# Performance work log

Hardware: AMD Instinct MI355X
Metric: run time of the kernel (lower is better)

The kernel has to match this reference:

```python
import jax, jax.numpy as jnp
import numpy as np

N = 50000
E = 800000
IN_DIM = 256
HID = 32
HEADS = 4
OUT_DIM = 40
NEG_SLOPE = 0.2


def gat_layer(x, src, dst, W, a_src, a_dst, b, n_nodes, heads, ch, concat):
    # x: [N, F_in], W: [F_in, heads*ch], a_src/a_dst: [heads, ch], b: [out]
    h = (x @ W).reshape(n_nodes, heads, ch)                 # [N,H,C]
    alpha_s = jnp.einsum('nhc,hc->nh', h, a_src)            # [N,H]
    alpha_d = jnp.einsum('nhc,hc->nh', h, a_dst)            # [N,H]
    e = jax.nn.leaky_relu(alpha_s[src] + alpha_d[dst], NEG_SLOPE)  # [E,H]
    # segment softmax over destination neighborhoods (self-loops guarantee nonempty)
    m = jax.ops.segment_max(e, dst, num_segments=n_nodes)   # [N,H]
    e = jnp.exp(e - m[dst])
    denom = jax.ops.segment_sum(e, dst, num_segments=n_nodes)
    alpha = e / (denom[dst] + 1e-16)                         # [E,H]
    msg = h[src] * alpha[:, :, None]                         # [E,H,C]
    out = jax.ops.segment_sum(msg, dst, num_segments=n_nodes)  # [N,H,C]
    out = out.reshape(n_nodes, heads * ch) if concat else out.mean(axis=1)
    return out + b


def setup_inputs() -> dict:
    key = jax.random.key(0)
    ks = jax.random.split(key, 10)
    x = jax.random.normal(ks[0], (N, IN_DIM), dtype=jnp.float32)
    edge_index = jax.random.randint(ks[1], (2, E), 0, N, dtype=jnp.int32)
    s1 = 1.0 / np.sqrt(IN_DIM)
    s2 = 1.0 / np.sqrt(HID * HEADS)
    return {
        'x': x,
        'edge_index': edge_index,
        'W1': jax.random.normal(ks[2], (IN_DIM, HEADS * HID), dtype=jnp.float32) * s1,
        'a_src1': jax.random.normal(ks[3], (HEADS, HID), dtype=jnp.float32) * s1,
        'a_dst1': jax.random.normal(ks[4], (HEADS, HID), dtype=jnp.float32) * s1,
        'b1': jnp.zeros((HEADS * HID,), dtype=jnp.float32),
        'W2': jax.random.normal(ks[5], (HEADS * HID, OUT_DIM), dtype=jnp.float32) * s2,
        'a_src2': jax.random.normal(ks[6], (1, OUT_DIM), dtype=jnp.float32) * s2,
        'a_dst2': jax.random.normal(ks[7], (1, OUT_DIM), dtype=jnp.float32) * s2,
        'b2': jnp.zeros((OUT_DIM,), dtype=jnp.float32),
    }


def reference(x, edge_index, W1, a_src1, a_dst1, b1, W2, a_src2, a_dst2, b2):
    # PyG GATConv adds self-loops by default
    loops = jnp.arange(N, dtype=edge_index.dtype)
    src = jnp.concatenate([edge_index[0], loops])
    dst = jnp.concatenate([edge_index[1], loops])
    h = gat_layer(x, src, dst, W1, a_src1, a_dst1, b1, N, HEADS, HID, True)
    h = jax.nn.relu(h)
    out = gat_layer(h, src, dst, W2, a_src2, a_dst2, b2, N, 1, OUT_DIM, False)
    return jax.nn.log_softmax(out, axis=1)
```

## Files before the change

### kernel.cpp

```cpp
#include <hip/hip_runtime.h>
#include <math.h>

#define N_NODES 50000
#define N_EDGES 800000
#define IN_DIM  256
#define F1      128
#define HEADS   4
#define OUT_DIM 40
#define NEG     0.2f

#define NB   391
#define CAP  3072
#define EB   4096
#define PREW 16
#define G1B  782

typedef __attribute__((ext_vector_type(8))) short short8;
typedef __attribute__((ext_vector_type(4))) float float4v;

__device__ __forceinline__ unsigned short f2bf(float f) {
  unsigned int u = __float_as_uint(f);
  u += 0x7FFF + ((u >> 16) & 1);
  return (unsigned short)(u >> 16);
}
__device__ __forceinline__ float bf2f(unsigned short h) {
  return __uint_as_float((unsigned int)h << 16);
}
__device__ __forceinline__ float bflo(unsigned int u) { return __uint_as_float(u << 16); }
__device__ __forceinline__ float bfhi(unsigned int u) { return __uint_as_float(u & 0xffff0000u); }

__device__ __forceinline__ float lrelu(float e) { return e > 0.f ? e : e * NEG; }

__device__ __forceinline__ void gload_lds16(const void* g, void* l) {
  __builtin_amdgcn_global_load_lds(
      (const __attribute__((address_space(1))) unsigned int*)g,
      (__attribute__((address_space(3))) unsigned int*)l, 16, 0, 0);
}

__global__ __launch_bounds__(256) void pre_kernel(const float* __restrict__ W1,
                                                  unsigned short* __restrict__ wHi,
                                                  unsigned short* __restrict__ wLo,
                                                  const int* __restrict__ ei,
                                                  int* __restrict__ gcnt,
                                                  int2* __restrict__ gbucket) {
  __shared__ int smem[EB * 2 + NB * 3];
  if (blockIdx.x < PREW) {
    int tid = blockIdx.x * 256 + threadIdx.x;
    int kk = tid >> 9;
    int rest = tid & 511;
    int t = rest >> 6;
    int lane = rest & 63;
    int q = lane >> 4;
    int ln = lane & 15;
    int n = t * 16 + ln;
    unsigned int hi[4], lo[4];
#pragma unroll
    for (int jj = 0; jj < 4; jj++) {
      unsigned short h0, h1, l0, l1;
      {
        float v = W1[(kk * 32 + q * 8 + jj * 2) * F1 + n];
        h0 = f2bf(v); l0 = f2bf(v - bf2f(h0));
      }
      {
        float v = W1[(kk * 32 + q * 8 + jj * 2 + 1) * F1 + n];
        h1 = f2bf(v); l1 = f2bf(v - bf2f(h1));
      }
      hi[jj] = (unsigned int)h0 | ((unsigned int)h1 << 16);
      lo[jj] = (unsigned int)l0 | ((unsigned int)l1 << 16);
    }
    size_t base = (size_t)tid * 8;
    *(uint4*)&wHi[base] = make_uint4(hi[0], hi[1], hi[2], hi[3]);
    *(uint4*)&wLo[base] = make_uint4(lo[0], lo[1], lo[2], lo[3]);
  } else {
    int* ls = smem;
    int* ld = smem + EB;
    int* lcnt = smem + 2 * EB;
    int* lcur = lcnt + NB;
    int* gbaseS = lcur + NB;
    int tid = threadIdx.x;
    size_t base = (size_t)(blockIdx.x - PREW) * EB;
    for (int t = tid; t < NB; t += 256) { lcnt[t] = 0; lcur[t] = 0; }
    __syncthreads();
#pragma unroll
    for (int l = 0; l < EB / 256; l++) {
      int li = l * 256 + tid;
      size_t idx = base + li;
      int s = 0, d = -1;
      if (idx < N_EDGES) {
        s = ei[idx];
        d = ei[N_EDGES + idx];
        atomicAdd(&lcnt[d >> 7], 1);
      }
      ls[li] = s;
      ld[li] = d;
    }
    __syncthreads();
    for (int t = tid; t < NB; t += 256) gbaseS[t] = atomicAdd(&gcnt[t], lcnt[t]);
    __syncthreads();
#pragma unroll
    for (int l = 0; l < EB / 256; l++) {
      int li = l * 256 + tid;
      int d = ld[li];
      if (d >= 0) {
        int b = d >> 7;
        int r = gbaseS[b] + atomicAdd(&lcur[b], 1);
        if (r >= CAP) r = CAP - 1;
        gbucket[(size_t)b * CAP + r] = make_int2(ls[li], d);
      }
    }
  }
}

__global__ __launch_bounds__(256) void mid_kernel(
    const float* __restrict__ x, const unsigned short* __restrict__ wHi,
    const unsigned short* __restrict__ wLo,
    const float* __restrict__ a_src, const float* __restrict__ a_dst,
    unsigned short* __restrict__ h1b, float* __restrict__ as1, float* __restrict__ ad1,
    const int2* __restrict__ gbucket, const int* __restrict__ gcnt,
    int* __restrict__ row_ptr, int* __restrict__ col) {
  __shared__ short8 smem[2048];
  if (blockIdx.x < G1B) {
    short8 (*Bsh)[1024] = (short8(*)[1024])smem;
    int bid = blockIdx.x;
    int tid = threadIdx.x;
    int w = tid >> 6;
    int lane = tid & 63;
    int q = lane >> 4;
    int ln = lane & 15;
    int rowBase = bid * 64 + w * 16;
    int rowA = rowBase + ln;
    int rowAc = rowA < N_NODES ? rowA : N_NODES - 1;
    float4v acc[8];
#pragma unroll
    for (int t = 0; t < 8; t++) acc[t] = (float4v){0.f, 0.f, 0.f, 0.f};
    const short8* bhp = (const short8*)wHi;
    const short8* blp = (const short8*)wLo;

    auto prefetch = [&](int kk, int buf) {
#pragma unroll
      for (int c = 0; c < 2; c++) {
        int chunk = w * 2 + c;
        gload_lds16(bhp + (size_t)kk * 512 + chunk * 64 + lane, &Bsh[buf][chunk * 64]);
        gload_lds16(blp + (size_t)kk * 512 + chunk * 64 + lane, &Bsh[buf][512 + chunk * 64]);
      }
    };

    const float4* xbase = (const float4*)(x + (size_t)rowAc * IN_DIM + q * 8);
    float4 a0 = xbase[0];
    float4 a1 = xbase[1];
    prefetch(0, 0);
    __syncthreads();

#pragma unroll 1
    for (int kk = 0; kk < 8; kk++) {
      int buf = kk & 1;
      if (kk < 7) prefetch(kk + 1, buf ^ 1);
      int kn = (kk < 7) ? kk + 1 : 7;
      float4 n0 = xbase[kn * 8];
      float4 n1 = xbase[kn * 8 + 1];
      float av[8] = {a0.x, a0.y, a0.z, a0.w, a1.x, a1.y, a1.z, a1.w};
      short8 ahi, alo;
#pragma unroll
      for (int j = 0; j < 8; j++) {
        unsigned short hh = f2bf(av[j]);
        ahi[j] = (short)hh;
        alo[j] = (short)f2bf(av[j] - bf2f(hh));
      }
      const short8* bs = &Bsh[buf][0];
#pragma unroll
      for (int t = 0; t < 8; t++) {
        short8 bh = bs[t * 64 + lane];
        short8 bl = bs[512 + t * 64 + lane];
        acc[t] = __builtin_amdgcn_mfma_f32_16x16x32_bf16(ahi, bh, acc[t], 0, 0, 0);
        acc[t] = __builtin_amdgcn_mfma_f32_16x16x32_bf16(ahi, bl, acc[t], 0, 0, 0);
        acc[t] = __builtin_amdgcn_mfma_f32_16x16x32_bf16(alo, bh, acc[t], 0, 0, 0);
      }
      a0 = n0;
      a1 = n1;
      if (kk < 7) __syncthreads();
    }

    float asv[8], adv[8];
#pragma unroll
    for (int t = 0; t < 8; t++) {
      asv[t] = a_src[t * 16 + ln];
      adv[t] = a_dst[t * 16 + ln];
    }
#pragma unroll
    for (int reg = 0; reg < 4; reg++) {
      int r = rowBase + q * 4 + reg;
      bool valid = (r < N_NODES);
      if (valid) {
#pragma unroll
        for (int t = 0; t < 8; t++)
          h1b[(size_t)r * F1 + t * 16 + ln] = f2bf(acc[t][reg]);
      }
#pragma unroll
      for (int h = 0; h < 4; h++) {
        float sa = acc[2 * h][reg] * asv[2 * h] + acc[2 * h + 1][reg] * asv[2 * h + 1];
        float sd = acc[2 * h][reg] * adv[2 * h] + acc[2 * h + 1][reg] * adv[2 * h + 1];
#pragma unroll
        for (int off = 1; off < 16; off <<= 1) {
          sa += __shfl_xor(sa, off);
          sd += __shfl_xor(sd, off);
        }
        if (ln == 0 && valid) {
          as1[r * 4 + h] = sa;
          ad1[r * 4 + h] = sd;
        }
      }
    }
  } else {
    int2* ent = (int2*)smem;
    int* hcnt = (int*)(ent + CAP);
    int* sc   = hcnt + 128;
    int* cur  = sc + 128;
    int* red  = cur + 128;
    int b = blockIdx.x - G1B;
    int tid = threadIdx.x;
    int cnt = gcnt[b]; if (cnt > CAP) cnt = CAP;
    if (tid < 128) hcnt[tid] = 0;
    int part = 0;
    for (int i = tid; i < b; i += 256) part += gcnt[i];
#pragma unroll
    for (int off = 32; off > 0; off >>= 1) part += __shfl_xor(part, off);
    if ((tid & 63) == 0) red[tid >> 6] = part;
    __syncthreads();
    int base = red[0] + red[1] + red[2] + red[3];
    for (int i = tid; i < cnt; i += 256) {
      int2 e = gbucket[(size_t)b * CAP + i];
      ent[i] = e;
      atomicAdd(&hcnt[e.y & 127], 1);
    }
    __syncthreads();
    if (tid < 128) sc[tid] = hcnt[tid];
    __syncthreads();
    for (int off = 1; off < 128; off <<= 1) {
      int t = 0;
      if (tid < 128 && tid >= off) t = sc[tid - off];
      __syncthreads();
      if (tid < 128) sc[tid] += t;
      __syncthreads();
    }
    if (tid < 128) {
      int excl = sc[tid] - hcnt[tid];
      cur[tid] = excl;
      int node = (b << 7) + tid;
      if (node < N_NODES) row_ptr[node] = base + excl;
    }
    if (b == 0 && tid == 0) row_ptr[N_NODES] = N_EDGES;
    __syncthreads();
    for (int i = tid; i < cnt; i += 256) {
      int2 e = ent[i];
      int r = atomicAdd(&cur[e.y & 127], 1);
      col[base + r] = e.x;
    }
  }
}

__global__ __launch_bounds__(256) void gather1_kernel(
    const unsigned short* __restrict__ h1b, const float* __restrict__ as1,
    const float* __restrict__ ad1, const float* __restrict__ b1,
    const int* __restrict__ row_ptr, const int* __restrict__ col,
    float* __restrict__ x2) {
  int wv = threadIdx.x >> 6;
  int n = blockIdx.x * 4 + wv;
  if (n >= N_NODES) return;
  int lane = threadIdx.x & 63;
  int start = row_ptr[n];
  int deg = row_ptr[n + 1] - start;
  int slot = lane >> 4;
  int lane16 = lane & 15;
  int head = lane16 >> 2;
  float adh = ad1[n * 4 + head];
  float4 accA = make_float4(0.f, 0.f, 0.f, 0.f);
  float4 accB = make_float4(0.f, 0.f, 0.f, 0.f);
  float dn = 0.f;
  int i = slot;
  for (; i + 4 <= deg; i += 8) {
    int sA = col[start + i];
    int sB = (i + 4 < deg) ? col[start + i + 4] : n;
    float eA = __expf(lrelu(as1[sA * 4 + head] + adh));
    float eB = __expf(lrelu(as1[sB * 4 + head] + adh));
    uint4 uA = *(const uint4*)(h1b + (size_t)sA * F1 + lane16 * 8);
    uint4 uB = *(const uint4*)(h1b + (size_t)sB * F1 + lane16 * 8);
    dn += eA + eB;
    accA.x += eA * bflo(uA.x); accA.y += eA * bfhi(uA.x);
    accA.z += eA * bflo(uA.y); accA.w += eA * bfhi(uA.y);
    accB.x += eA * bflo(uA.z); accB.y += eA * bfhi(uA.z);
    accB.z += eA * bflo(uA.w); accB.w += eA * bfhi(uA.w);
    accA.x += eB * bflo(uB.x); accA.y += eB * bfhi(uB.x);
    accA.z += eB * bflo(uB.y); accA.w += eB * bfhi(uB.y);
    accB.x += eB * bflo(uB.z); accB.y += eB * bfhi(uB.z);
    accB.z += eB * bflo(uB.w); accB.w += eB * bfhi(uB.w);
  }
  if (i <= deg) {
    int s = (i < deg) ? col[start + i] : n;
    float e = __expf(lrelu(as1[s * 4 + head] + adh));
    uint4 u = *(const uint4*)(h1b + (size_t)s * F1 + lane16 * 8);
    dn += e;
    accA.x += e * bflo(u.x); accA.y += e * bfhi(u.x);
    accA.z += e * bflo(u.y); accA.w += e * bfhi(u.y);
    accB.x += e * bflo(u.z); accB.y += e * bfhi(u.z);
    accB.z += e * bflo(u.w); accB.w += e * bfhi(u.w);
  }
#pragma unroll
  for (int off = 16; off <= 32; off <<= 1) {
    accA.x += __shfl_xor(accA.x, off); accA.y += __shfl_xor(accA.y, off);
    accA.z += __shfl_xor(accA.z, off); accA.w += __shfl_xor(accA.w, off);
    accB.x += __shfl_xor(accB.x, off); accB.y += __shfl_xor(accB.y, off);
    accB.z += __shfl_xor(accB.z, off); accB.w += __shfl_xor(accB.w, off);
    dn += __shfl_xor(dn, off);
  }
  if (slot == 0) {
    float rsh = 1.f / (dn + 1e-16f);
    float4 bA = *(const float4*)&b1[lane16 * 8];
    float4 bB = *(const float4*)&b1[lane16 * 8 + 4];
    float4 oA, oB;
    oA.x = fmaxf(accA.x * rsh + bA.x, 0.f); oA.y = fmaxf(accA.y * rsh + bA.y, 0.f);
    oA.z = fmaxf(accA.z * rsh + bA.z, 0.f); oA.w = fmaxf(accA.w * rsh + bA.w, 0.f);
    oB.x = fmaxf(accB.x * rsh + bB.x, 0.f); oB.y = fmaxf(accB.y * rsh + bB.y, 0.f);
    oB.z = fmaxf(accB.z * rsh + bB.z, 0.f); oB.w = fmaxf(accB.w * rsh + bB.w, 0.f);
    *(float4*)&x2[(size_t)n * F1 + lane16 * 8] = oA;
    *(float4*)&x2[(size_t)n * F1 + lane16 * 8 + 4] = oB;
  }
}

__global__ __launch_bounds__(256) void gemm2_kernel(
    const float* __restrict__ x2, const float* __restrict__ W2,
    const float* __restrict__ asv, const float* __restrict__ adv,
    unsigned short* __restrict__ h2b, float* __restrict__ as2, float* __restrict__ ad2) {
  __shared__ float xs[64][132];
  __shared__ float W2s[128][44];
  __shared__ float asv_s[40], adv_s[40];
  int tid = threadIdx.x;
  int bm = blockIdx.x * 64;
#pragma unroll
  for (int l = 0; l < 8; l++) {
    int idx = tid + l * 256;
    int r = idx >> 5;
    int c4 = (idx & 31) << 2;
    float4 v = make_float4(0.f, 0.f, 0.f, 0.f);
    if (bm + r < N_NODES) v = *(const float4*)&x2[(size_t)(bm + r) * F1 + c4];
    *(float4*)&xs[r][c4] = v;
  }
#pragma unroll
  for (int l = 0; l < 5; l++) {
    int idx = tid + l * 256;
    int k = idx / 10;
    int c4 = (idx - k * 10) * 4;
    *(float4*)&W2s[k][c4] = *(const float4*)&W2[k * OUT_DIM + c4];
  }
  if (tid < OUT_DIM) { asv_s[tid] = asv[tid]; adv_s[tid] = adv[tid]; }
  __syncthreads();
  int r = tid >> 2;
  int cb = (tid & 3) * 10;
  float acc[10] = {0.f};
  for (int k = 0; k < F1; k++) {
    float xv = xs[r][k];
#pragma unroll
    for (int c = 0; c < 10; c++) acc[c] += xv * W2s[k][cb + c];
  }
  int grow = bm + r;
  float sa = 0.f, sd = 0.f;
#pragma unroll
  for (int c = 0; c < 10; c++) {
    sa += acc[c] * asv_s[cb + c];
    sd += acc[c] * adv_s[cb + c];
  }
#pragma unroll
  for (int off = 1; off < 4; off <<= 1) {
    sa += __shfl_xor(sa, off);
    sd += __shfl_xor(sd, off);
  }
  if (grow < N_NODES) {
#pragma unroll
    for (int c = 0; c < 10; c += 2) {
      unsigned int p = ((unsigned int)f2bf(acc[c + 1]) << 16) | f2bf(acc[c]);
      *(unsigned int*)&h2b[(size_t)grow * OUT_DIM + cb + c] = p;
    }
    if ((tid & 3) == 0) { as2[grow] = sa; ad2[grow] = sd; }
  }
}

__global__ __launch_bounds__(256) void gather2_kernel(
    const unsigned short* __restrict__ h2b, const float* __restrict__ as2,
    const float* __restrict__ ad2, const float* __restrict__ b2,
    const int* __restrict__ row_ptr, const int* __restrict__ col,
    float* __restrict__ out) {
  int wv = threadIdx.x >> 6;
  int n = blockIdx.x * 4 + wv;
  if (n >= N_NODES) return;
  int lane = threadIdx.x & 63;
  int start = row_ptr[n];
  int deg = row_ptr[n + 1] - start;
  float adh = ad2[n];
  int slot = lane / 5;
  int c = lane - slot * 5;
  float4 accA = make_float4(0.f, 0.f, 0.f, 0.f);
  float4 accB = make_float4(0.f, 0.f, 0.f, 0.f);
  float dn = 0.f;
  if (slot < 12) {
    for (int i = slot; i <= deg; i += 12) {
      int src = (i < deg) ? col[start + i] : n;
      float e = __expf(lrelu(as2[src] + adh));
      uint4 u = *(const uint4*)(h2b + (size_t)src * OUT_DIM + c * 8);
      dn += e;
      accA.x += e * bflo(u.x); accA.y += e * bfhi(u.x);
      accA.z += e * bflo(u.y); accA.w += e * bfhi(u.y);
      accB.x += e * bflo(u.z); accB.y += e * bfhi(u.z);
      accB.z += e * bflo(u.w); accB.w += e * bfhi(u.w);
    }
  }
  float v[9] = {accA.x, accA.y, accA.z, accA.w, accB.x, accB.y, accB.z, accB.w, dn};
#pragma unroll
  for (int k = 0; k < 9; k++) v[k] += __shfl(v[k], lane + 30);
#pragma unroll
  for (int k = 0; k < 9; k++) v[k] += __shfl(v[k], lane + 15);
  {
    float t1[9], t2[9];
#pragma unroll
    for (int k = 0; k < 9; k++) t1[k] = __shfl(v[k], lane + 5);
#pragma unroll
    for (int k = 0; k < 9; k++) t2[k] = __shfl(v[k], lane + 10);
#pragma unroll
    for (int k = 0; k < 9; k++) v[k] += t1[k] + t2[k];
  }
  bool owner = (slot == 0);
  float vals[8];
  float lmax = -1e30f, lsum = 0.f;
  if (owner) {
    float rs = 1.f / (v[8] + 1e-16f);
#pragma unroll
    for (int k = 0; k < 8; k++) {
      vals[k] = v[k] * rs + b2[c * 8 + k];
      lmax = fmaxf(lmax, vals[k]);
    }
  }
  float gmax = lmax;
#pragma unroll
  for (int off = 32; off > 0; off >>= 1) gmax = fmaxf(gmax, __shfl_xor(gmax, off));
  if (owner) {
#pragma unroll
    for (int k = 0; k < 8; k++) lsum += __expf(vals[k] - gmax);
  }
#pragma unroll
  for (int off = 32; off > 0; off >>= 1) lsum += __shfl_xor(lsum, off);
  if (owner) {
    float lse = gmax + __logf(lsum);
    float4 oA = make_float4(vals[0] - lse, vals[1] - lse, vals[2] - lse, vals[3] - lse);
    float4 oB = make_float4(vals[4] - lse, vals[5] - lse, vals[6] - lse, vals[7] - lse);
    *(float4*)&out[(size_t)n * OUT_DIM + c * 8] = oA;
    *(float4*)&out[(size_t)n * OUT_DIM + c * 8 + 4] = oB;
  }
}

extern "C" void kernel_launch(void* const* d_in, const int* in_sizes, int n_in,
                              void* d_out, int out_size, void* d_ws, size_t ws_size,
                              hipStream_t stream) {
  const float* x      = (const float*)d_in[0];
  const int*   ei     = (const int*)d_in[1];
  const float* W1     = (const float*)d_in[2];
  const float* a_src1 = (const float*)d_in[3];
  const float* a_dst1 = (const float*)d_in[4];
  const float* b1     = (const float*)d_in[5];
  const float* W2     = (const float*)d_in[6];
  const float* a_src2 = (const float*)d_in[7];
  const float* a_dst2 = (const float*)d_in[8];
  const float* b2     = (const float*)d_in[9];
  float* out = (float*)d_out;

  char* ws = (char*)d_ws;
  size_t off = 0;
  auto alloc = [&](size_t bytes) -> void* {
    void* p = ws + off;
    off += (bytes + 255) & ~(size_t)255;
    return p;
  };
  unsigned short* h1b = (unsigned short*)alloc((size_t)N_NODES * F1 * 2);
  unsigned short* h2b = (unsigned short*)alloc((size_t)N_NODES * OUT_DIM * 2);
  unsigned short* wHi = (unsigned short*)alloc((size_t)IN_DIM * F1 * 2);
  unsigned short* wLo = (unsigned short*)alloc((size_t)IN_DIM * F1 * 2);
  float* as1    = (float*)alloc((size_t)N_NODES * HEADS * 4);
  float* ad1    = (float*)alloc((size_t)N_NODES * HEADS * 4);
  float* x2     = (float*)alloc((size_t)N_NODES * F1 * 4);
  float* as2    = (float*)alloc((size_t)N_NODES * 4);
  float* ad2    = (float*)alloc((size_t)N_NODES * 4);
  int* row_ptr  = (int*)alloc((size_t)(N_NODES + 1) * 4);
  int* col      = (int*)alloc((size_t)N_EDGES * 4);
  int* gcnt     = (int*)alloc((size_t)NB * 4);
  int2* gbucket = (int2*)alloc((size_t)NB * CAP * 8);

  hipMemsetAsync(gcnt, 0, (size_t)NB * 4, stream);
  pre_kernel<<<PREW + (N_EDGES + EB - 1) / EB, 256, 0, stream>>>(W1, wHi, wLo, ei, gcnt, gbucket);
  mid_kernel<<<G1B + NB, 256, 0, stream>>>(x, wHi, wLo, a_src1, a_dst1, h1b, as1, ad1,
                                           gbucket, gcnt, row_ptr, col);
  gather1_kernel<<<(N_NODES + 3) / 4, 256, 0, stream>>>(h1b, as1, ad1, b1, row_ptr, col, x2);

  gemm2_kernel<<<(N_NODES + 63) / 64, 256, 0, stream>>>(x2, W2, a_src2, a_dst2, h2b, as2, ad2);
  gather2_kernel<<<(N_NODES + 3) / 4, 256, 0, stream>>>(h2b, as2, ad2, b2, row_ptr, col, out);
}
```

Baseline: 233.2 us.

## Fuse layer-2 linear projection into layer-1 gather kernel, drop x2 buffer

Layer-1 aggregation now goes straight into the layer-2 projection inside the gather kernel. Each wavefront stages its aggregated 128-wide row in shared memory and computes the 40 outputs plus the attention scalars against a transposed W2 held in shared memory. This removes the separate gemm2 launch and the fp32 x2 round trip to global memory. In exchange, every block reloads and transposes all of W2 into LDS, uses only 40 of 64 lanes in the dot product, and the bounds check is dropped, which relies on N being divisible by 4.

```diff
diff --git a/kernel.cpp b/kernel.cpp
--- a/kernel.cpp
+++ b/kernel.cpp
@@ -262,11 +262,22 @@
     const unsigned short* __restrict__ h1b, const float* __restrict__ as1,
     const float* __restrict__ ad1, const float* __restrict__ b1,
     const int* __restrict__ row_ptr, const int* __restrict__ col,
-    float* __restrict__ x2) {
-  int wv = threadIdx.x >> 6;
+    const float* __restrict__ W2, const float* __restrict__ a2s,
+    const float* __restrict__ a2d,
+    unsigned short* __restrict__ h2b, float* __restrict__ as2,
+    float* __restrict__ ad2) {
+  __shared__ float W2T[OUT_DIM][132];
+  __shared__ float xs[4][F1];
+  int tid = threadIdx.x;
+  for (int idx = tid; idx < OUT_DIM * F1; idx += 256) {
+    int c = idx >> 7;
+    int k = idx & 127;
+    W2T[c][k] = W2[k * OUT_DIM + c];
+  }
+  __syncthreads();
+  int wv = tid >> 6;
   int n = blockIdx.x * 4 + wv;
-  if (n >= N_NODES) return;
-  int lane = threadIdx.x & 63;
+  int lane = tid & 63;
   int start = row_ptr[n];
   int deg = row_ptr[n + 1] - start;
   int slot = lane >> 4;
@@ -312,74 +323,46 @@
     accB.z += __shfl_xor(accB.z, off); accB.w += __shfl_xor(accB.w, off);
     dn += __shfl_xor(dn, off);
   }
+  float rsh = 1.f / (dn + 1e-16f);
+  float4 bA = *(const float4*)&b1[lane16 * 8];
+  float4 bB = *(const float4*)&b1[lane16 * 8 + 4];
+  float4 oA, oB;
+  oA.x = fmaxf(accA.x * rsh + bA.x, 0.f); oA.y = fmaxf(accA.y * rsh + bA.y, 0.f);
+  oA.z = fmaxf(accA.z * rsh + bA.z, 0.f); oA.w = fmaxf(accA.w * rsh + bA.w, 0.f);
+  oB.x = fmaxf(accB.x * rsh + bB.x, 0.f); oB.y = fmaxf(accB.y * rsh + bB.y, 0.f);
+  oB.z = fmaxf(accB.z * rsh + bB.z, 0.f); oB.w = fmaxf(accB.w * rsh + bB.w, 0.f);
   if (slot == 0) {
-    float rsh = 1.f / (dn + 1e-16f);
-    float4 bA = *(const float4*)&b1[lane16 * 8];
-    float4 bB = *(const float4*)&b1[lane16 * 8 + 4];
-    float4 oA, oB;
-    oA.x = fmaxf(accA.x * rsh + bA.x, 0.f); oA.y = fmaxf(accA.y * rsh + bA.y, 0.f);
-    oA.z = fmaxf(accA.z * rsh + bA.z, 0.f); oA.w = fmaxf(accA.w * rsh + bA.w, 0.f);
-    oB.x = fmaxf(accB.x * rsh + bB.x, 0.f); oB.y = fmaxf(accB.y * rsh + bB.y, 0.f);
-    oB.z = fmaxf(accB.z * rsh + bB.z, 0.f); oB.w = fmaxf(accB.w * rsh + bB.w, 0.f);
-    *(float4*)&x2[(size_t)n * F1 + lane16 * 8] = oA;
-    *(float4*)&x2[(size_t)n * F1 + lane16 * 8 + 4] = oB;
-  }
-}
-
-__global__ __launch_bounds__(256) void gemm2_kernel(
-    const float* __restrict__ x2, const float* __restrict__ W2,
-    const float* __restrict__ asv, const float* __restrict__ adv,
-    unsigned short* __restrict__ h2b, float* __restrict__ as2, float* __restrict__ ad2) {
-  __shared__ float xs[64][132];
-  __shared__ float W2s[128][44];
-  __shared__ float asv_s[40], adv_s[40];
-  int tid = threadIdx.x;
-  int bm = blockIdx.x * 64;
-#pragma unroll
-  for (int l = 0; l < 8; l++) {
-    int idx = tid + l * 256;
-    int r = idx >> 5;
-    int c4 = (idx & 31) << 2;
-    float4 v = make_float4(0.f, 0.f, 0.f, 0.f);
-    if (bm + r < N_NODES) v = *(const float4*)&x2[(size_t)(bm + r) * F1 + c4];
-    *(float4*)&xs[r][c4] = v;
-  }
-#pragma unroll
-  for (int l = 0; l < 5; l++) {
-    int idx = tid + l * 256;
-    int k = idx / 10;
-    int c4 = (idx - k * 10) * 4;
-    *(float4*)&W2s[k][c4] = *(const float4*)&W2[k * OUT_DIM + c4];
-  }
-  if (tid < OUT_DIM) { asv_s[tid] = asv[tid]; adv_s[tid] = adv[tid]; }
-  __syncthreads();
-  int r = tid >> 2;
-  int cb = (tid & 3) * 10;
-  float acc[10] = {0.f};
-  for (int k = 0; k < F1; k++) {
-    float xv = xs[r][k];
-#pragma unroll
-    for (int c = 0; c < 10; c++) acc[c] += xv * W2s[k][cb + c];
-  }
-  int grow = bm + r;
-  float sa = 0.f, sd = 0.f;
-#pragma unroll
-  for (int c = 0; c < 10; c++) {
-    sa += acc[c] * asv_s[cb + c];
-    sd += acc[c] * adv_s[cb + c];
-  }
-#pragma unroll
-  for (int off = 1; off < 4; off <<= 1) {
+    *(float4*)&xs[wv][lane16 * 8] = oA;
+    *(float4*)&xs[wv][lane16 * 8 + 4] = oB;
+  }
+  int c = lane;
+  const float4* wrow = (const float4*)&W2T[(c < OUT_DIM) ? c : 0][0];
+  const float4* xrow = (const float4*)&xs[wv][0];
+  float h2v = 0.f;
+#pragma unroll
+  for (int kb = 0; kb < F1 / 4; kb++) {
+    float4 wv4 = wrow[kb];
+    float4 xv4 = xrow[kb];
+    h2v += xv4.x * wv4.x;
+    h2v += xv4.y * wv4.y;
+    h2v += xv4.z * wv4.z;
+    h2v += xv4.w * wv4.w;
+  }
+  if (c >= OUT_DIM) h2v = 0.f;
+  float a2sv = (c < OUT_DIM) ? a2s[c] : 0.f;
+  float a2dv = (c < OUT_DIM) ? a2d[c] : 0.f;
+  float sa = h2v * a2sv;
+  float sd = h2v * a2dv;
+#pragma unroll
+  for (int off = 1; off < 64; off <<= 1) {
     sa += __shfl_xor(sa, off);
     sd += __shfl_xor(sd, off);
   }
-  if (grow < N_NODES) {
-#pragma unroll
-    for (int c = 0; c < 10; c += 2) {
-      unsigned int p = ((unsigned int)f2bf(acc[c + 1]) << 16) | f2bf(acc[c]);
-      *(unsigned int*)&h2b[(size_t)grow * OUT_DIM + cb + c] = p;
-    }
-    if ((tid & 3) == 0) { as2[grow] = sa; ad2[grow] = sd; }
+  if (lane == 0) { as2[n] = sa; ad2[n] = sd; }
+  unsigned int hu = (unsigned int)f2bf(h2v);
+  unsigned int hn = (unsigned int)__shfl((int)hu, lane + 1);
+  if ((c & 1) == 0 && c < OUT_DIM) {
+    *(unsigned int*)&h2b[(size_t)n * OUT_DIM + c] = hu | (hn << 16);
   }
 }
 
@@ -483,7 +466,6 @@
   unsigned short* wLo = (unsigned short*)alloc((size_t)IN_DIM * F1 * 2);
   float* as1    = (float*)alloc((size_t)N_NODES * HEADS * 4);
   float* ad1    = (float*)alloc((size_t)N_NODES * HEADS * 4);
-  float* x2     = (float*)alloc((size_t)N_NODES * F1 * 4);
   float* as2    = (float*)alloc((size_t)N_NODES * 4);
   float* ad2    = (float*)alloc((size_t)N_NODES * 4);
   int* row_ptr  = (int*)alloc((size_t)(N_NODES + 1) * 4);
@@ -495,8 +477,7 @@
   pre_kernel<<<PREW + (N_EDGES + EB - 1) / EB, 256, 0, stream>>>(W1, wHi, wLo, ei, gcnt, gbucket);
   mid_kernel<<<G1B + NB, 256, 0, stream>>>(x, wHi, wLo, a_src1, a_dst1, h1b, as1, ad1,
                                            gbucket, gcnt, row_ptr, col);
-  gather1_kernel<<<(N_NODES + 3) / 4, 256, 0, stream>>>(h1b, as1, ad1, b1, row_ptr, col, x2);
-
-  gemm2_kernel<<<(N_NODES + 63) / 64, 256, 0, stream>>>(x2, W2, a_src2, a_dst2, h2b, as2, ad2);
-  gather2_kernel<<<(N_NODES + 3) / 4, 256, 0, stream>>>(h2b, as2, ad2, b2, row_ptr, col, out);
-}
+  gather1_kernel<<<N_NODES / 4, 256, 0, stream>>>(h1b, as1, ad1, b1, row_ptr, col,
+                                                  W2, a_src2, a_dst2, h2b, as2, ad2);
+  gather2_kernel<<<N_NODES / 4, 256, 0, stream>>>(h2b, as2, ad2, b2, row_ptr, col, out);
+}
```

After: 474.1 us. 2.03x slower.

## Split mid_kernel GEMM columns across 8 waves and halve pre_kernel edge block

Applied to the files above, without the earlier changes.

The fused GEMM/CSR-build kernel now runs 512-thread blocks. Each pair of waves splits the 128 output columns in half, so every wave keeps 4 accumulators instead of 8 and loads only one B chunk per stage. The CSR-build branch strides over 512 threads and reduces over 8 partial sums. The pre_kernel edge block size is halved to spread binning over more blocks. The aim is lower register pressure and more waves in flight to hide memory latency. The cost is that each A row is loaded and split into bf16 hi/lo twice per block.

```diff
diff --git a/kernel.cpp b/kernel.cpp
--- a/kernel.cpp
+++ b/kernel.cpp
@@ -11,7 +11,7 @@
 
 #define NB   391
 #define CAP  3072
-#define EB   4096
+#define EB   2048
 #define PREW 16
 #define G1B  782
 
@@ -111,7 +111,7 @@
   }
 }
 
-__global__ __launch_bounds__(256) void mid_kernel(
+__global__ __launch_bounds__(512, 6) void mid_kernel(
     const float* __restrict__ x, const unsigned short* __restrict__ wHi,
     const unsigned short* __restrict__ wLo,
     const float* __restrict__ a_src, const float* __restrict__ a_dst,
@@ -125,24 +125,23 @@
     int tid = threadIdx.x;
     int w = tid >> 6;
     int lane = tid & 63;
+    int ch = w >> 2;
+    int w4 = w & 3;
     int q = lane >> 4;
     int ln = lane & 15;
-    int rowBase = bid * 64 + w * 16;
+    int rowBase = bid * 64 + w4 * 16;
     int rowA = rowBase + ln;
     int rowAc = rowA < N_NODES ? rowA : N_NODES - 1;
-    float4v acc[8];
-#pragma unroll
-    for (int t = 0; t < 8; t++) acc[t] = (float4v){0.f, 0.f, 0.f, 0.f};
+    float4v acc[4];
+#pragma unroll
+    for (int t = 0; t < 4; t++) acc[t] = (float4v){0.f, 0.f, 0.f, 0.f};
     const short8* bhp = (const short8*)wHi;
     const short8* blp = (const short8*)wLo;
 
     auto prefetch = [&](int kk, int buf) {
-#pragma unroll
-      for (int c = 0; c < 2; c++) {
-        int chunk = w * 2 + c;
-        gload_lds16(bhp + (size_t)kk * 512 + chunk * 64 + lane, &Bsh[buf][chunk * 64]);
-        gload_lds16(blp + (size_t)kk * 512 + chunk * 64 + lane, &Bsh[buf][512 + chunk * 64]);
-      }
+      int chunk = w;
+      gload_lds16(bhp + (size_t)kk * 512 + chunk * 64 + lane, &Bsh[buf][chunk * 64]);
+      gload_lds16(blp + (size_t)kk * 512 + chunk * 64 + lane, &Bsh[buf][512 + chunk * 64]);
     };
 
     const float4* xbase = (const float4*)(x + (size_t)rowAc * IN_DIM + q * 8);
@@ -168,9 +167,10 @@
       }
       const short8* bs = &Bsh[buf][0];
 #pragma unroll
-      for (int t = 0; t < 8; t++) {
-        short8 bh = bs[t * 64 + lane];
-        short8 bl = bs[512 + t * 64 + lane];
+      for (int t = 0; t < 4; t++) {
+        int te = ch * 4 + t;
+        short8 bh = bs[te * 64 + lane];
+        short8 bl = bs[512 + te * 64 + lane];
         acc[t] = __builtin_amdgcn_mfma_f32_16x16x32_bf16(ahi, bh, acc[t], 0, 0, 0);
         acc[t] = __builtin_amdgcn_mfma_f32_16x16x32_bf16(ahi, bl, acc[t], 0, 0, 0);
         acc[t] = __builtin_amdgcn_mfma_f32_16x16x32_bf16(alo, bh, acc[t], 0, 0, 0);
@@ -180,11 +180,11 @@
       if (kk < 7) __syncthreads();
     }
 
-    float asv[8], adv[8];
-#pragma unroll
-    for (int t = 0; t < 8; t++) {
-      asv[t] = a_src[t * 16 + ln];
-      adv[t] = a_dst[t * 16 + ln];
+    float asv[4], adv[4];
+#pragma unroll
+    for (int t = 0; t < 4; t++) {
+      asv[t] = a_src[(ch * 4 + t) * 16 + ln];
+      adv[t] = a_dst[(ch * 4 + t) * 16 + ln];
     }
 #pragma unroll
     for (int reg = 0; reg < 4; reg++) {
@@ -192,21 +192,21 @@
       bool valid = (r < N_NODES);
       if (valid) {
 #pragma unroll
-        for (int t = 0; t < 8; t++)
-          h1b[(size_t)r * F1 + t * 16 + ln] = f2bf(acc[t][reg]);
-      }
-#pragma unroll
-      for (int h = 0; h < 4; h++) {
-        float sa = acc[2 * h][reg] * asv[2 * h] + acc[2 * h + 1][reg] * asv[2 * h + 1];
-        float sd = acc[2 * h][reg] * adv[2 * h] + acc[2 * h + 1][reg] * adv[2 * h + 1];
+        for (int t = 0; t < 4; t++)
+          h1b[(size_t)r * F1 + (ch * 4 + t) * 16 + ln] = f2bf(acc[t][reg]);
+      }
+#pragma unroll
+      for (int hh = 0; hh < 2; hh++) {
+        float sa = acc[2 * hh][reg] * asv[2 * hh] + acc[2 * hh + 1][reg] * asv[2 * hh + 1];
+        float sd = acc[2 * hh][reg] * adv[2 * hh] + acc[2 * hh + 1][reg] * adv[2 * hh + 1];
 #pragma unroll
         for (int off = 1; off < 16; off <<= 1) {
           sa += __shfl_xor(sa, off);
           sd += __shfl_xor(sd, off);
         }
         if (ln == 0 && valid) {
-          as1[r * 4 + h] = sa;
-          ad1[r * 4 + h] = sd;
+          as1[r * 4 + ch * 2 + hh] = sa;
+          ad1[r * 4 + ch * 2 + hh] = sd;
         }
       }
     }
@@ -221,13 +221,13 @@
     int cnt = gcnt[b]; if (cnt > CAP) cnt = CAP;
     if (tid < 128) hcnt[tid] = 0;
     int part = 0;
-    for (int i = tid; i < b; i += 256) part += gcnt[i];
+    for (int i = tid; i < b; i += 512) part += gcnt[i];
 #pragma unroll
     for (int off = 32; off > 0; off >>= 1) part += __shfl_xor(part, off);
     if ((tid & 63) == 0) red[tid >> 6] = part;
     __syncthreads();
-    int base = red[0] + red[1] + red[2] + red[3];
-    for (int i = tid; i < cnt; i += 256) {
+    int base = red[0] + red[1] + red[2] + red[3] + red[4] + red[5] + red[6] + red[7];
+    for (int i = tid; i < cnt; i += 512) {
       int2 e = gbucket[(size_t)b * CAP + i];
       ent[i] = e;
       atomicAdd(&hcnt[e.y & 127], 1);
@@ -250,7 +250,7 @@
     }
     if (b == 0 && tid == 0) row_ptr[N_NODES] = N_EDGES;
     __syncthreads();
-    for (int i = tid; i < cnt; i += 256) {
+    for (int i = tid; i < cnt; i += 512) {
       int2 e = ent[i];
       int r = atomicAdd(&cur[e.y & 127], 1);
       col[base + r] = e.x;
@@ -493,7 +493,7 @@
 
   hipMemsetAsync(gcnt, 0, (size_t)NB * 4, stream);
   pre_kernel<<<PREW + (N_EDGES + EB - 1) / EB, 256, 0, stream>>>(W1, wHi, wLo, ei, gcnt, gbucket);
-  mid_kernel<<<G1B + NB, 256, 0, stream>>>(x, wHi, wLo, a_src1, a_dst1, h1b, as1, ad1,
+  mid_kernel<<<G1B + NB, 512, 0, stream>>>(x, wHi, wLo, a_src1, a_dst1, h1b, as1, ad1,
                                            gbucket, gcnt, row_ptr, col);
   gather1_kernel<<<(N_NODES + 3) / 4, 256, 0, stream>>>(h1b, as1, ad1, b1, row_ptr, col, x2);
 
```

Measured after the change: 236.8 us. About the same (+1.5%).
